# Optimization experiments

Measured on AMD Instinct MI355X. Metric: run time of the kernel, lower is better.

## Reference

```python
import jax, jax.numpy as jnp
import numpy as np

RHO = 1.0
EPSILON = 0.1
N_ITERS = 5
EPS = 1e-08


def setup_inputs() -> dict:
    key = jax.random.key(0)
    k1, k2, k3 = jax.random.split(key, 3)
    B, H, M, N, D = 16, 16, 256, 576, 1024
    # student cross-attention weights: positive, rows roughly sum to 1 (post-softmax in the real model)
    sa = jax.random.uniform(k1, (B, H, M, N), dtype=jnp.float32) + 1e-3
    student_attn = sa / sa.sum(axis=-1, keepdims=True)
    visual_feats = jax.random.normal(k2, (B, N, D), dtype=jnp.float32)
    text_feats = jax.random.normal(k3, (B, M, D), dtype=jnp.float32)
    text_mask = jnp.ones((B, M), dtype=jnp.float32)
    return {"student_attn": student_attn, "visual_feats": visual_feats,
            "text_feats": text_feats, "text_mask": text_mask}


def _l2norm(x):
    return x / jnp.sqrt(jnp.sum(x * x, axis=-1, keepdims=True) + 1e-12)


def _teacher_plan(x, y, y_mask):
    # x: (B,N,D) visual, y: (B,M,D) text, y_mask: (B,M)
    B, N, D = x.shape
    M = y.shape[1]
    x_n = _l2norm(x)
    y_n = _l2norm(y)
    cost = 1.0 - jnp.einsum('bmd,bnd->bmn', y_n, x_n)          # (B,M,N)
    mu = jnp.full((B, N, 1), 1.0 / N, dtype=x.dtype)            # visual marginal (column vec)
    nu = (y_mask / (jnp.sum(y_mask, axis=1, keepdims=True) + EPS))[:, :, None]  # (B,M,1)
    K = jnp.exp(-cost / EPSILON)                                # (B,M,N)
    fi = RHO / (RHO + EPSILON)
    u = jnp.ones((B, M, 1), dtype=x.dtype)
    v = jnp.ones((B, N, 1), dtype=x.dtype)
    for _ in range(N_ITERS):
        Kv = jnp.einsum('bmn,bnk->bmk', K, v)                   # (B,M,1)
        u = (nu / (Kv + EPS)) ** fi
        Ktu = jnp.einsum('bmn,bmk->bnk', K, u)                  # (B,N,1)
        v = (mu / (Ktu + EPS)) ** fi
    P = u * K * jnp.swapaxes(v, 1, 2)                           # (B,M,N)
    return P / (jnp.sum(P, axis=-1, keepdims=True) + EPS)


def reference(student_attn, visual_feats, text_feats, text_mask):
    teacher = jax.lax.stop_gradient(_teacher_plan(visual_feats, text_feats, text_mask))
    teacher = teacher[:, None, :, :]                            # (B,1,M,N)
    loss = -jnp.sum(teacher * jnp.log(student_attn + EPS), axis=-1)  # (B,H,M)
    loss = loss * text_mask[:, None, :]
    return jnp.mean(loss)
```

## Files before the change

kernel.cpp:

```cpp
#include <hip/hip_runtime.h>
#include <math.h>

#define B_ 16
#define H_ 16
#define M_ 256
#define N_ 576
#define D_ 1024
#define BK 64
#define LDS_STRIDE (BK + 8)
#define NROWS (B_ * N_ + B_ * M_)

constexpr float EPS_ = 1e-8f;
constexpr float FI_ = 0.90909090909090906f;

typedef __bf16 bf16x8 __attribute__((ext_vector_type(8)));
typedef float f32x4 __attribute__((ext_vector_type(4)));

__device__ __forceinline__ float wave_reduce(float v) {
#pragma unroll
  for (int o = 32; o > 0; o >>= 1) v += __shfl_down(v, o, 64);
  return v;
}

__device__ __forceinline__ unsigned short f2bf(float f) {
  union { float f; unsigned u; } a; a.f = f;
  unsigned r = a.u + 0x7fff + ((a.u >> 16) & 1);
  return (unsigned short)(r >> 16);
}

__device__ __forceinline__ float bf2f(unsigned short u) {
  union { unsigned u; float f; } a; a.u = ((unsigned)u) << 16;
  return a.f;
}

__global__ __launch_bounds__(256) void sumlog_kernel(const float* __restrict__ student,
                                                     float* __restrict__ SL) {
  const int m = blockIdx.x;
  const int b = blockIdx.y;
  const int t = threadIdx.x;
  if (t >= N_ / 4) return;
  const float* st = student + ((size_t)b * H_ * M_ + m) * N_ + t * 4;
  float4 acc = {0.f, 0.f, 0.f, 0.f};
#pragma unroll
  for (int h = 0; h < H_; ++h) {
    float4 s4 = *(const float4*)&st[(size_t)h * M_ * N_];
    acc.x += __logf(s4.x + EPS_);
    acc.y += __logf(s4.y + EPS_);
    acc.z += __logf(s4.z + EPS_);
    acc.w += __logf(s4.w + EPS_);
  }
  *(float4*)&SL[((size_t)b * M_ + m) * N_ + t * 4] = acc;
}

__global__ __launch_bounds__(256) void prep_kernel(const float* __restrict__ vis,
                                                   const float* __restrict__ txt,
                                                   const float* __restrict__ mask,
                                                   unsigned short* __restrict__ xb,
                                                   unsigned short* __restrict__ yb,
                                                   float* __restrict__ masksum) {
  const int bid = blockIdx.x;
  const int lane = threadIdx.x & 63;
  if (bid < NROWS / 4) {
    int wave = bid * 4 + (threadIdx.x >> 6);
    const float* src;
    unsigned short* dst;
    if (wave < B_ * N_) {
      src = vis + (size_t)wave * D_;
      dst = xb + (size_t)wave * D_;
    } else {
      int r = wave - B_ * N_;
      src = txt + (size_t)r * D_;
      dst = yb + (size_t)r * D_;
    }
    float4 v[4];
    float s = 0.f;
#pragma unroll
    for (int it = 0; it < 4; ++it) {
      v[it] = *(const float4*)&src[it * 256 + lane * 4];
      s += v[it].x * v[it].x + v[it].y * v[it].y + v[it].z * v[it].z + v[it].w * v[it].w;
    }
    s = wave_reduce(s);
    s = __shfl(s, 0, 64);
    float inv = rsqrtf(s + 1e-12f);
#pragma unroll
    for (int it = 0; it < 4; ++it) {
      ushort4 pk;
      pk.x = f2bf(v[it].x * inv);
      pk.y = f2bf(v[it].y * inv);
      pk.z = f2bf(v[it].z * inv);
      pk.w = f2bf(v[it].w * inv);
      *(ushort4*)&dst[it * 256 + lane * 4] = pk;
    }
  } else {
    int b = (bid - NROWS / 4) * 4 + (threadIdx.x >> 6);
    float4 mv = *(const float4*)&mask[b * M_ + lane * 4];
    float s = wave_reduce(mv.x + mv.y + mv.z + mv.w);
    if (lane == 0) masksum[b] = s;
  }
}

__global__ __launch_bounds__(256) void gemm_k_mfma(const unsigned short* __restrict__ xb,
                                                   const unsigned short* __restrict__ yb,
                                                   unsigned short* __restrict__ Kw) {
  __shared__ unsigned short As[64][LDS_STRIDE];
  __shared__ unsigned short Bs[64][LDS_STRIDE];
  const int b = blockIdx.z;
  const int m0 = blockIdx.y * 64;
  const int n0 = blockIdx.x * 64;
  const unsigned short* Y = yb + (size_t)b * M_ * D_;
  const unsigned short* X = xb + (size_t)b * N_ * D_;
  const int t = threadIdx.x;
  const int lane = t & 63;
  const int w = t >> 6;
  const int wm = (w & 1) * 32;
  const int wn = (w >> 1) * 32;
  const int lr = t >> 3;
  const int lc = (t & 7) * 8;
  const int fr = lane & 15;
  const int fk = (lane >> 4) * 8;

  f32x4 acc[2][2] = {};
  for (int k0 = 0; k0 < D_; k0 += BK) {
#pragma unroll
    for (int p = 0; p < 2; ++p) {
      *(uint4*)&As[lr + 32 * p][lc] = *(const uint4*)&Y[(size_t)(m0 + lr + 32 * p) * D_ + k0 + lc];
      *(uint4*)&Bs[lr + 32 * p][lc] = *(const uint4*)&X[(size_t)(n0 + lr + 32 * p) * D_ + k0 + lc];
    }
    __syncthreads();
#pragma unroll
    for (int ks = 0; ks < BK; ks += 32) {
      bf16x8 a[2], bfr[2];
#pragma unroll
      for (int i = 0; i < 2; ++i) {
        a[i] = *(const bf16x8*)&As[wm + i * 16 + fr][ks + fk];
        bfr[i] = *(const bf16x8*)&Bs[wn + i * 16 + fr][ks + fk];
      }
#pragma unroll
      for (int i = 0; i < 2; ++i)
#pragma unroll
        for (int j = 0; j < 2; ++j)
          acc[i][j] = __builtin_amdgcn_mfma_f32_16x16x32_bf16(a[i], bfr[j], acc[i][j], 0, 0, 0);
    }
    __syncthreads();
  }

  const int cm = (lane >> 4) * 4;
  const int cn = lane & 15;
#pragma unroll
  for (int i = 0; i < 2; ++i)
#pragma unroll
    for (int j = 0; j < 2; ++j)
#pragma unroll
      for (int rg = 0; rg < 4; ++rg) {
        int m = m0 + wm + i * 16 + cm + rg;
        int n = n0 + wn + j * 16 + cn;
        Kw[((size_t)b * M_ + m) * N_ + n] = f2bf(expf(10.f * (acc[i][j][rg] - 1.f)));
      }
}


__global__ __launch_bounds__(256) void sink_u_first(const unsigned short* __restrict__ Kw,
                                                    const float* __restrict__ mask,
                                                    const float* __restrict__ masksum,
                                                    float* __restrict__ u) {
  const int b = blockIdx.y;
  const int row = blockIdx.x * 4 + (threadIdx.x >> 6);
  const int lane = threadIdx.x & 63;
  const unsigned short* rowp = Kw + ((size_t)b * M_ + row) * N_;
  float s = 0.f;
#pragma unroll
  for (int k = 0; k < 9; ++k) s += bf2f(rowp[lane + 64 * k]);
  s = wave_reduce(s);
  if (lane == 0) {
    int idx = b * M_ + row;
    float nu = mask[idx] / (masksum[b] + EPS_);
    u[idx] = powf(nu / (s + EPS_), FI_);
  }
}

__global__ __launch_bounds__(256) void sink_u(const unsigned short* __restrict__ Kw,
                                              const float* __restrict__ v,
                                              const float* __restrict__ mask,
                                              const float* __restrict__ masksum,
                                              float* __restrict__ u) {
  const int b = blockIdx.y;
  const int row = blockIdx.x * 4 + (threadIdx.x >> 6);
  const int lane = threadIdx.x & 63;
  const unsigned short* rowp = Kw + ((size_t)b * M_ + row) * N_;
  const float* vb = v + b * N_;
  float s = 0.f;
#pragma unroll
  for (int k = 0; k < 9; ++k) s += bf2f(rowp[lane + 64 * k]) * vb[lane + 64 * k];
  s = wave_reduce(s);
  if (lane == 0) {
    int idx = b * M_ + row;
    float nu = mask[idx] / (masksum[b] + EPS_);
    u[idx] = powf(nu / (s + EPS_), FI_);
  }
}

__global__ __launch_bounds__(256) void sink_v(const unsigned short* __restrict__ Kw,
                                              const float* __restrict__ u,
                                              float* __restrict__ v) {
  __shared__ float part[4][64];
  const int b = blockIdx.y;
  const int n0 = blockIdx.x * 64;
  const int col = n0 + (threadIdx.x & 63);
  const int g = threadIdx.x >> 6;
  const unsigned short* Kb = Kw + (size_t)b * M_ * N_;
  const float* ub = u + b * M_;
  float s = 0.f;
#pragma unroll 8
  for (int m = g * 64; m < (g + 1) * 64; ++m) s += bf2f(Kb[(size_t)m * N_ + col]) * ub[m];
  part[g][threadIdx.x & 63] = s;
  __syncthreads();
  if (threadIdx.x < 64) {
    float tot = part[0][threadIdx.x] + part[1][threadIdx.x] +
                part[2][threadIdx.x] + part[3][threadIdx.x];
    v[b * N_ + n0 + threadIdx.x] = powf((1.f / (float)N_) / (tot + EPS_), FI_);
  }
}

__global__ __launch_bounds__(256) void finloss_kernel(const unsigned short* __restrict__ Kw,
                                                      const float* __restrict__ SL,
                                                      const float* __restrict__ v,
                                                      const float* __restrict__ mask,
                                                      float* __restrict__ partial) {
  __shared__ float red[2][4];
  const int m = blockIdx.x;
  const int b = blockIdx.y;
  const int t = threadIdx.x;
  float s1 = 0.f, s2 = 0.f;
  if (t < N_ / 4) {
    const unsigned short* kp = Kw + ((size_t)b * M_ + m) * N_ + t * 4;
    ushort4 k4 = *(const ushort4*)kp;
    float4 v4 = *(const float4*)&v[b * N_ + t * 4];
    float4 sl4 = *(const float4*)&SL[((size_t)b * M_ + m) * N_ + t * 4];
    float kv0 = bf2f(k4.x) * v4.x, kv1 = bf2f(k4.y) * v4.y;
    float kv2 = bf2f(k4.z) * v4.z, kv3 = bf2f(k4.w) * v4.w;
    s1 = kv0 + kv1 + kv2 + kv3;
    s2 = kv0 * sl4.x + kv1 * sl4.y + kv2 * sl4.z + kv3 * sl4.w;
  }
  s1 = wave_reduce(s1);
  s2 = wave_reduce(s2);
  if ((t & 63) == 0) { red[0][t >> 6] = s1; red[1][t >> 6] = s2; }
  __syncthreads();
  if (t == 0) {
    float S1 = red[0][0] + red[0][1] + red[0][2] + red[0][3];
    float S2 = red[1][0] + red[1][1] + red[1][2] + red[1][3];
    int row = b * M_ + m;
    partial[row] = -mask[row] * S2 / ((S1 + EPS_) * (float)(B_ * H_ * M_));
  }
}

__global__ __launch_bounds__(256) void reduce_kernel(const float* __restrict__ partial,
                                                     float* __restrict__ out) {
  __shared__ float red[4];
  float s = 0.f;
  for (int i = threadIdx.x; i < B_ * M_; i += 256) s += partial[i];
  s = wave_reduce(s);
  if ((threadIdx.x & 63) == 0) red[threadIdx.x >> 6] = s;
  __syncthreads();
  if (threadIdx.x == 0) out[0] = red[0] + red[1] + red[2] + red[3];
}

extern "C" void kernel_launch(void* const* d_in, const int* in_sizes, int n_in,
                              void* d_out, int out_size, void* d_ws, size_t ws_size,
                              hipStream_t stream) {
  const float* student = (const float*)d_in[0];
  const float* vis = (const float*)d_in[1];
  const float* txt = (const float*)d_in[2];
  const float* mask = (const float*)d_in[3];
  float* out = (float*)d_out;

  char* p = (char*)d_ws;
  unsigned short* Kb = (unsigned short*)p; p += (size_t)B_ * M_ * N_ * 2;
  unsigned short* xb = (unsigned short*)p; p += (size_t)B_ * N_ * D_ * 2;
  unsigned short* yb = (unsigned short*)p; p += (size_t)B_ * M_ * D_ * 2;
  float* SL = (float*)p;      p += (size_t)B_ * M_ * N_ * 4;
  float* vv = (float*)p;      p += B_ * N_ * 4;
  float* uu = (float*)p;      p += B_ * M_ * 4;
  float* msum = (float*)p;    p += B_ * 4;
  float* partial = (float*)p; p += B_ * M_ * 4;

  sumlog_kernel<<<dim3(M_, B_), 256, 0, stream>>>(student, SL);

  prep_kernel<<<NROWS / 4 + 4, 256, 0, stream>>>(vis, txt, mask, xb, yb, msum);
  gemm_k_mfma<<<dim3(N_ / 64, M_ / 64, B_), 256, 0, stream>>>(xb, yb, Kb);

  sink_u_first<<<dim3(M_ / 4, B_), 256, 0, stream>>>(Kb, mask, msum, uu);
  sink_v<<<dim3(N_ / 64, B_), 256, 0, stream>>>(Kb, uu, vv);
  for (int it = 1; it < 5; ++it) {
    sink_u<<<dim3(M_ / 4, B_), 256, 0, stream>>>(Kb, vv, mask, msum, uu);
    sink_v<<<dim3(N_ / 64, B_), 256, 0, stream>>>(Kb, uu, vv);
  }

  finloss_kernel<<<dim3(M_, B_), 256, 0, stream>>>(Kb, SL, vv, mask, partial);
  reduce_kernel<<<1, 256, 0, stream>>>(partial, out);
}
```

Measured before the change: 335.6 us.

## Fuse Sinkhorn iterations and loss into one per-batch register-resident kernel

```diff
diff --git a/kernel.cpp b/kernel.cpp
--- a/kernel.cpp
+++ b/kernel.cpp
@@ -28,18 +28,16 @@
   return (unsigned short)(r >> 16);
 }
 
-__device__ __forceinline__ float bf2f(unsigned short u) {
-  union { unsigned u; float f; } a; a.u = ((unsigned)u) << 16;
+__device__ __forceinline__ float bits2f(unsigned u) {
+  union { unsigned u; float f; } a; a.u = u;
   return a.f;
 }
 
 __global__ __launch_bounds__(256) void sumlog_kernel(const float* __restrict__ student,
                                                      float* __restrict__ SL) {
-  const int m = blockIdx.x;
   const int b = blockIdx.y;
-  const int t = threadIdx.x;
-  if (t >= N_ / 4) return;
-  const float* st = student + ((size_t)b * H_ * M_ + m) * N_ + t * 4;
+  const size_t mn4 = (size_t)blockIdx.x * 256 + threadIdx.x;
+  const float* st = student + (size_t)b * H_ * M_ * N_ + mn4 * 4;
   float4 acc = {0.f, 0.f, 0.f, 0.f};
 #pragma unroll
   for (int h = 0; h < H_; ++h) {
@@ -49,53 +47,43 @@
     acc.z += __logf(s4.z + EPS_);
     acc.w += __logf(s4.w + EPS_);
   }
-  *(float4*)&SL[((size_t)b * M_ + m) * N_ + t * 4] = acc;
+  *(float4*)&SL[(size_t)b * M_ * N_ + mn4 * 4] = acc;
 }
 
 __global__ __launch_bounds__(256) void prep_kernel(const float* __restrict__ vis,
                                                    const float* __restrict__ txt,
-                                                   const float* __restrict__ mask,
                                                    unsigned short* __restrict__ xb,
-                                                   unsigned short* __restrict__ yb,
-                                                   float* __restrict__ masksum) {
-  const int bid = blockIdx.x;
+                                                   unsigned short* __restrict__ yb) {
   const int lane = threadIdx.x & 63;
-  if (bid < NROWS / 4) {
-    int wave = bid * 4 + (threadIdx.x >> 6);
-    const float* src;
-    unsigned short* dst;
-    if (wave < B_ * N_) {
-      src = vis + (size_t)wave * D_;
-      dst = xb + (size_t)wave * D_;
-    } else {
-      int r = wave - B_ * N_;
-      src = txt + (size_t)r * D_;
-      dst = yb + (size_t)r * D_;
-    }
-    float4 v[4];
-    float s = 0.f;
-#pragma unroll
-    for (int it = 0; it < 4; ++it) {
-      v[it] = *(const float4*)&src[it * 256 + lane * 4];
-      s += v[it].x * v[it].x + v[it].y * v[it].y + v[it].z * v[it].z + v[it].w * v[it].w;
-    }
-    s = wave_reduce(s);
-    s = __shfl(s, 0, 64);
-    float inv = rsqrtf(s + 1e-12f);
-#pragma unroll
-    for (int it = 0; it < 4; ++it) {
-      ushort4 pk;
-      pk.x = f2bf(v[it].x * inv);
-      pk.y = f2bf(v[it].y * inv);
-      pk.z = f2bf(v[it].z * inv);
-      pk.w = f2bf(v[it].w * inv);
-      *(ushort4*)&dst[it * 256 + lane * 4] = pk;
-    }
+  int wave = blockIdx.x * 4 + (threadIdx.x >> 6);
+  const float* src;
+  unsigned short* dst;
+  if (wave < B_ * N_) {
+    src = vis + (size_t)wave * D_;
+    dst = xb + (size_t)wave * D_;
   } else {
-    int b = (bid - NROWS / 4) * 4 + (threadIdx.x >> 6);
-    float4 mv = *(const float4*)&mask[b * M_ + lane * 4];
-    float s = wave_reduce(mv.x + mv.y + mv.z + mv.w);
-    if (lane == 0) masksum[b] = s;
+    int r = wave - B_ * N_;
+    src = txt + (size_t)r * D_;
+    dst = yb + (size_t)r * D_;
+  }
+  float4 v[4];
+  float s = 0.f;
+#pragma unroll
+  for (int it = 0; it < 4; ++it) {
+    v[it] = *(const float4*)&src[it * 256 + lane * 4];
+    s += v[it].x * v[it].x + v[it].y * v[it].y + v[it].z * v[it].z + v[it].w * v[it].w;
+  }
+  s = wave_reduce(s);
+  s = __shfl(s, 0, 64);
+  float inv = rsqrtf(s + 1e-12f);
+#pragma unroll
+  for (int it = 0; it < 4; ++it) {
+    ushort4 pk;
+    pk.x = f2bf(v[it].x * inv);
+    pk.y = f2bf(v[it].y * inv);
+    pk.z = f2bf(v[it].z * inv);
+    pk.w = f2bf(v[it].w * inv);
+    *(ushort4*)&dst[it * 256 + lane * 4] = pk;
   }
 }
 
@@ -158,110 +146,102 @@
       }
 }
 
-
-__global__ __launch_bounds__(256) void sink_u_first(const unsigned short* __restrict__ Kw,
-                                                    const float* __restrict__ mask,
-                                                    const float* __restrict__ masksum,
-                                                    float* __restrict__ u) {
-  const int b = blockIdx.y;
-  const int row = blockIdx.x * 4 + (threadIdx.x >> 6);
-  const int lane = threadIdx.x & 63;
-  const unsigned short* rowp = Kw + ((size_t)b * M_ + row) * N_;
-  float s = 0.f;
-#pragma unroll
-  for (int k = 0; k < 9; ++k) s += bf2f(rowp[lane + 64 * k]);
-  s = wave_reduce(s);
-  if (lane == 0) {
-    int idx = b * M_ + row;
-    float nu = mask[idx] / (masksum[b] + EPS_);
-    u[idx] = powf(nu / (s + EPS_), FI_);
-  }
-}
-
-__global__ __launch_bounds__(256) void sink_u(const unsigned short* __restrict__ Kw,
-                                              const float* __restrict__ v,
-                                              const float* __restrict__ mask,
-                                              const float* __restrict__ masksum,
-                                              float* __restrict__ u) {
-  const int b = blockIdx.y;
-  const int row = blockIdx.x * 4 + (threadIdx.x >> 6);
-  const int lane = threadIdx.x & 63;
-  const unsigned short* rowp = Kw + ((size_t)b * M_ + row) * N_;
-  const float* vb = v + b * N_;
-  float s = 0.f;
-#pragma unroll
-  for (int k = 0; k < 9; ++k) s += bf2f(rowp[lane + 64 * k]) * vb[lane + 64 * k];
-  s = wave_reduce(s);
-  if (lane == 0) {
-    int idx = b * M_ + row;
-    float nu = mask[idx] / (masksum[b] + EPS_);
-    u[idx] = powf(nu / (s + EPS_), FI_);
-  }
-}
-
-__global__ __launch_bounds__(256) void sink_v(const unsigned short* __restrict__ Kw,
-                                              const float* __restrict__ u,
-                                              float* __restrict__ v) {
-  __shared__ float part[4][64];
-  const int b = blockIdx.y;
-  const int n0 = blockIdx.x * 64;
-  const int col = n0 + (threadIdx.x & 63);
-  const int g = threadIdx.x >> 6;
+__global__ __launch_bounds__(1024) void sinkloss_kernel(const unsigned short* __restrict__ Kw,
+                                                        const float* __restrict__ SL,
+                                                        const float* __restrict__ mask,
+                                                        float* __restrict__ out) {
+  __shared__ float partv[16][N_];
+  __shared__ float sv[N_];
+  __shared__ float su[M_];
+  __shared__ float snu[M_];
+  __shared__ float smask[M_];
+  __shared__ float srow[M_];
+  __shared__ float sred[16];
+  const int b = blockIdx.x;
+  const int t = threadIdx.x;
+  const int lane = t & 63;
+  const int w = t >> 6;
+  const int r0 = w * 16;
   const unsigned short* Kb = Kw + (size_t)b * M_ * N_;
-  const float* ub = u + b * M_;
-  float s = 0.f;
-#pragma unroll 8
-  for (int m = g * 64; m < (g + 1) * 64; ++m) s += bf2f(Kb[(size_t)m * N_ + col]) * ub[m];
-  part[g][threadIdx.x & 63] = s;
+
+  float mv = (t < M_) ? mask[b * M_ + t] : 0.f;
+  float wsum = wave_reduce(mv);
+  if (t < M_ && lane == 0) sred[w] = wsum;
+  if (t < N_) sv[t] = 1.f;
+  if (t < M_) smask[t] = mv;
   __syncthreads();
-  if (threadIdx.x < 64) {
-    float tot = part[0][threadIdx.x] + part[1][threadIdx.x] +
-                part[2][threadIdx.x] + part[3][threadIdx.x];
-    v[b * N_ + n0 + threadIdx.x] = powf((1.f / (float)N_) / (tot + EPS_), FI_);
-  }
-}
-
-__global__ __launch_bounds__(256) void finloss_kernel(const unsigned short* __restrict__ Kw,
-                                                      const float* __restrict__ SL,
-                                                      const float* __restrict__ v,
-                                                      const float* __restrict__ mask,
-                                                      float* __restrict__ partial) {
-  __shared__ float red[2][4];
-  const int m = blockIdx.x;
-  const int b = blockIdx.y;
-  const int t = threadIdx.x;
-  float s1 = 0.f, s2 = 0.f;
-  if (t < N_ / 4) {
-    const unsigned short* kp = Kw + ((size_t)b * M_ + m) * N_ + t * 4;
-    ushort4 k4 = *(const ushort4*)kp;
-    float4 v4 = *(const float4*)&v[b * N_ + t * 4];
-    float4 sl4 = *(const float4*)&SL[((size_t)b * M_ + m) * N_ + t * 4];
-    float kv0 = bf2f(k4.x) * v4.x, kv1 = bf2f(k4.y) * v4.y;
-    float kv2 = bf2f(k4.z) * v4.z, kv3 = bf2f(k4.w) * v4.w;
-    s1 = kv0 + kv1 + kv2 + kv3;
-    s2 = kv0 * sl4.x + kv1 * sl4.y + kv2 * sl4.z + kv3 * sl4.w;
-  }
-  s1 = wave_reduce(s1);
-  s2 = wave_reduce(s2);
-  if ((t & 63) == 0) { red[0][t >> 6] = s1; red[1][t >> 6] = s2; }
+  if (t < M_) {
+    float msum = sred[0] + sred[1] + sred[2] + sred[3];
+    snu[t] = mv / (msum + EPS_);
+  }
+
+  unsigned kreg[9][8];
+#pragma unroll
+  for (int j = 0; j < 9; ++j)
+#pragma unroll
+    for (int p = 0; p < 8; ++p) {
+      unsigned lo = Kb[(size_t)(r0 + 2 * p) * N_ + lane + 64 * j];
+      unsigned hi = Kb[(size_t)(r0 + 2 * p + 1) * N_ + lane + 64 * j];
+      kreg[j][p] = lo | (hi << 16);
+    }
+#define KVAL(j, i) bits2f(((i) & 1) ? (kreg[j][(i) >> 1] & 0xffff0000u) : (kreg[j][(i) >> 1] << 16))
+
+  __syncthreads();
+
+  for (int it = 0; it < 5; ++it) {
+#pragma unroll
+    for (int i = 0; i < 16; ++i) {
+      float s = 0.f;
+#pragma unroll
+      for (int j = 0; j < 9; ++j) s += KVAL(j, i) * sv[lane + 64 * j];
+      s = wave_reduce(s);
+      if (lane == 0) srow[r0 + i] = s;
+    }
+    __syncthreads();
+    if (t < M_) su[t] = powf(snu[t] / (srow[t] + EPS_), FI_);
+    __syncthreads();
+#pragma unroll
+    for (int j = 0; j < 9; ++j) {
+      float s = 0.f;
+#pragma unroll
+      for (int i = 0; i < 16; ++i) s += KVAL(j, i) * su[r0 + i];
+      partv[w][lane + 64 * j] = s;
+    }
+    __syncthreads();
+    if (t < N_) {
+      float s = 0.f;
+#pragma unroll
+      for (int ww = 0; ww < 16; ++ww) s += partv[ww][t];
+      sv[t] = powf((1.f / (float)N_) / (s + EPS_), FI_);
+    }
+    __syncthreads();
+  }
+
+  float acc = 0.f;
+#pragma unroll
+  for (int i = 0; i < 16; ++i) {
+    const int r = r0 + i;
+    const float* slp = SL + ((size_t)b * M_ + r) * N_;
+    float s1 = 0.f, s2 = 0.f;
+#pragma unroll
+    for (int j = 0; j < 9; ++j) {
+      float kv = KVAL(j, i) * sv[lane + 64 * j];
+      s1 += kv;
+      s2 += kv * slp[lane + 64 * j];
+    }
+    s1 = wave_reduce(s1);
+    s2 = wave_reduce(s2);
+    if (lane == 0) acc -= smask[r] * s2 / (s1 + EPS_);
+  }
+  if (lane == 0) sred[w] = acc;
   __syncthreads();
   if (t == 0) {
-    float S1 = red[0][0] + red[0][1] + red[0][2] + red[0][3];
-    float S2 = red[1][0] + red[1][1] + red[1][2] + red[1][3];
-    int row = b * M_ + m;
-    partial[row] = -mask[row] * S2 / ((S1 + EPS_) * (float)(B_ * H_ * M_));
-  }
-}
-
-__global__ __launch_bounds__(256) void reduce_kernel(const float* __restrict__ partial,
-                                                     float* __restrict__ out) {
-  __shared__ float red[4];
-  float s = 0.f;
-  for (int i = threadIdx.x; i < B_ * M_; i += 256) s += partial[i];
-  s = wave_reduce(s);
-  if ((threadIdx.x & 63) == 0) red[threadIdx.x >> 6] = s;
-  __syncthreads();
-  if (threadIdx.x == 0) out[0] = red[0] + red[1] + red[2] + red[3];
+    float tot = 0.f;
+#pragma unroll
+    for (int ww = 0; ww < 16; ++ww) tot += sred[ww];
+    atomicAdd(out, tot * (1.f / ((float)B_ * H_ * M_)));
+  }
+#undef KVAL
 }
 
 extern "C" void kernel_launch(void* const* d_in, const int* in_sizes, int n_in,
@@ -278,23 +258,10 @@
   unsigned short* xb = (unsigned short*)p; p += (size_t)B_ * N_ * D_ * 2;
   unsigned short* yb = (unsigned short*)p; p += (size_t)B_ * M_ * D_ * 2;
   float* SL = (float*)p;      p += (size_t)B_ * M_ * N_ * 4;
-  float* vv = (float*)p;      p += B_ * N_ * 4;
-  float* uu = (float*)p;      p += B_ * M_ * 4;
-  float* msum = (float*)p;    p += B_ * 4;
-  float* partial = (float*)p; p += B_ * M_ * 4;
-
-  sumlog_kernel<<<dim3(M_, B_), 256, 0, stream>>>(student, SL);
-
-  prep_kernel<<<NROWS / 4 + 4, 256, 0, stream>>>(vis, txt, mask, xb, yb, msum);
+
+  hipMemsetAsync(d_out, 0, sizeof(float), stream);
+  sumlog_kernel<<<dim3(M_ * N_ / 4 / 256, B_), 256, 0, stream>>>(student, SL);
+  prep_kernel<<<NROWS / 4, 256, 0, stream>>>(vis, txt, xb, yb);
   gemm_k_mfma<<<dim3(N_ / 64, M_ / 64, B_), 256, 0, stream>>>(xb, yb, Kb);
-
-  sink_u_first<<<dim3(M_ / 4, B_), 256, 0, stream>>>(Kb, mask, msum, uu);
-  sink_v<<<dim3(N_ / 64, B_), 256, 0, stream>>>(Kb, uu, vv);
-  for (int it = 1; it < 5; ++it) {
-    sink_u<<<dim3(M_ / 4, B_), 256, 0, stream>>>(Kb, vv, mask, msum, uu);
-    sink_v<<<dim3(N_ / 64, B_), 256, 0, stream>>>(Kb, uu, vv);
-  }
-
-  finloss_kernel<<<dim3(M_, B_), 256, 0, stream>>>(Kb, SL, vv, mask, partial);
-  reduce_kernel<<<1, 256, 0, stream>>>(partial, out);
-}
+  sinkloss_kernel<<<B_, 1024, 0, stream>>>(Kb, SL, mask, out);
+}
```

Measured after the change: 402.4 us. 19.9% more time.
